# Performance work log

Measured on AMD Instinct MI355X. Metric: run time of the kernel, lower is better.

The kernel has to match this reference:

```python
import jax, jax.numpy as jnp
import numpy as np
import math

N_HEAD = 8
FACTOR = 1


def setup_inputs() -> dict:
    key = jax.random.key(0)
    kq, kk, kv = jax.random.split(key, 3)
    B, L, D = 16, 2048, 512
    return {
        "queries": jax.random.normal(kq, (B, L, D), dtype=jnp.float32),
        "keys": jax.random.normal(kk, (B, L, D), dtype=jnp.float32),
        "values": jax.random.normal(kv, (B, L, D), dtype=jnp.float32),
    }


def _autocorrelation(queries, keys, values):
    B, L, D = queries.shape
    H = N_HEAD
    E = D // H
    top_k = int(FACTOR * math.log(L))  # static: L is a Python int

    # (B,L,H,E) -> (B,H,E,L)
    q = queries.reshape(B, L, H, E).transpose(0, 2, 3, 1)
    k = keys.reshape(B, L, H, E).transpose(0, 2, 3, 1)
    v = values.reshape(B, L, H, E).transpose(0, 2, 3, 1)

    # period-based dependencies via FFT cross-correlation
    qf = jnp.fft.rfft(q, axis=-1)
    kf = jnp.fft.rfft(k, axis=-1)
    corr = jnp.fft.irfft(qf * jnp.conj(kf), n=L, axis=-1)  # (B,H,E,L)

    # time-delay aggregation (training path)
    mean_value = corr.mean(axis=(1, 2))                      # (B,L)
    index = jax.lax.top_k(mean_value.mean(axis=0), top_k)[1]  # (top_k,)
    weights = mean_value[:, index]                            # (B,top_k)
    tmp_corr = jax.nn.softmax(weights, axis=-1)               # (B,top_k)

    # roll values by each top-k delay and combine with softmax weights
    patterns = jax.vmap(lambda d: jnp.roll(v, -d, axis=-1))(index)  # (k,B,H,E,L)
    V = jnp.einsum('kbhel,bk->bhel', patterns, tmp_corr)            # (B,H,E,L)

    out = V.transpose(0, 3, 1, 2).reshape(B, L, D)
    corr_out = corr.transpose(0, 3, 1, 2).reshape(B, L, D)
    return out, corr_out


def reference(queries, keys, values):
    return _autocorrelation(queries, keys, values)
```

## Files before the change

kernel.cpp:

```cpp
#include <hip/hip_runtime.h>
#include <math.h>

#define B_  16
#define L_  2048
#define D_  512
#define K_  7
#define Q_  (B_*L_*D_)

__global__ __launch_bounds__(256) void kA(const float* __restrict__ q,
                                          const float* __restrict__ k,
                                          float* __restrict__ qT,
                                          float* __restrict__ kT) {
  __shared__ float tq[32][33];
  __shared__ float tk[32][33];
  const int l0 = blockIdx.x * 32, d0 = blockIdx.y * 32, b = blockIdx.z;
  const int tx = threadIdx.x, ty = threadIdx.y;
  const size_t ibase = (size_t)b * L_ * D_;
#pragma unroll
  for (int j = 0; j < 4; ++j) {
    const int l = l0 + ty + 8 * j;
    tq[ty + 8 * j][tx] = q[ibase + (size_t)l * D_ + d0 + tx];
    tk[ty + 8 * j][tx] = k[ibase + (size_t)l * D_ + d0 + tx];
  }
  __syncthreads();
  const size_t obase = (size_t)b * D_ * L_;
#pragma unroll
  for (int j = 0; j < 4; ++j) {
    const int d = d0 + ty + 8 * j;
    qT[obase + (size_t)d * L_ + l0 + tx] = tq[tx][ty + 8 * j];
    kT[obase + (size_t)d * L_ + l0 + tx] = tk[tx][ty + 8 * j];
  }
}

struct cf { float r, i; };
__device__ __forceinline__ cf cadd(cf a, cf b){ return {a.r+b.r, a.i+b.i}; }
__device__ __forceinline__ cf csub(cf a, cf b){ return {a.r-b.r, a.i-b.i}; }
__device__ __forceinline__ cf cmul(cf a, cf b){ return {a.r*b.r - a.i*b.i, a.r*b.i + a.i*b.r}; }
template<bool INV> __device__ __forceinline__ cf rot90(cf x){
  return INV ? cf{-x.i, x.r} : cf{x.i, -x.r};
}
__device__ __forceinline__ int swzA(int a){ return a ^ (((a >> 6) & 7) << 3); }
__device__ __forceinline__ int swzB(int a){ return a ^ (((a >> 3) ^ (a >> 6)) & 7); }

template<bool INV>
__device__ __forceinline__ void dft8(cf a[8], cf b[8]) {
  const float H = 0.70710678118654752440f;
  cf t0 = cadd(a[0],a[4]), t1 = cadd(a[1],a[5]), t2 = cadd(a[2],a[6]), t3 = cadd(a[3],a[7]);
  cf u0 = csub(a[0],a[4]), u1 = csub(a[1],a[5]), u2 = csub(a[2],a[6]), u3 = csub(a[3],a[7]);
  const cf w1 = INV ? cf{H,  H} : cf{ H, -H};
  const cf w3 = INV ? cf{-H, H} : cf{-H, -H};
  u1 = cmul(u1, w1);
  u2 = rot90<INV>(u2);
  u3 = cmul(u3, w3);
  { cf s0 = cadd(t0,t2), s1 = csub(t0,t2), s2 = cadd(t1,t3), s3 = rot90<INV>(csub(t1,t3));
    b[0]=cadd(s0,s2); b[4]=csub(s0,s2); b[2]=cadd(s1,s3); b[6]=csub(s1,s3); }
  { cf s0 = cadd(u0,u2), s1 = csub(u0,u2), s2 = cadd(u1,u3), s3 = rot90<INV>(csub(u1,u3));
    b[1]=cadd(s0,s2); b[5]=csub(s0,s2); b[3]=cadd(s1,s3); b[7]=csub(s1,s3); }
}

template<int LOG2S, bool INV, bool SRC_A>
__device__ __forceinline__ void pass8(const float* __restrict__ sr,
                                      const float* __restrict__ si,
                                      float* __restrict__ dr,
                                      float* __restrict__ di, int tid) {
  const int p = tid >> LOG2S;
  cf a[8], b[8];
#pragma unroll
  for (int l = 0; l < 8; ++l) {
    const int ix = tid + (l << 8);
    const int rs = SRC_A ? swzA(ix) : swzB(ix);
    a[l].r = sr[rs]; a[l].i = si[rs];
  }
  dft8<INV>(a, b);
  const float ANG = -0.0030679615757712823f;
  float sn, cs;
  __sincosf(ANG * (float)(p << LOG2S), &sn, &cs);
  if (INV) sn = -sn;
  const cf w1{cs, sn};
  cf w = w1;
  b[1] = cmul(b[1], w);
#pragma unroll
  for (int k = 2; k < 8; ++k) { w = cmul(w, w1); b[k] = cmul(b[k], w); }
  const int wb = tid + 7 * (p << LOG2S);
#pragma unroll
  for (int k = 0; k < 8; ++k) {
    const int ix = wb + (k << LOG2S);
    const int ws = SRC_A ? swzB(ix) : swzA(ix);
    dr[ws] = b[k].r; di[ws] = b[k].i;
  }
}

template<bool INV>
__device__ __forceinline__ void pass4_final(const float* __restrict__ sr,
                                            const float* __restrict__ si,
                                            float* __restrict__ dr,
                                            float* __restrict__ di, int tid) {
#pragma unroll
  for (int h = 0; h < 2; ++h) {
    const int j = tid + (h << 8);
    const int r0 = swzB(j), r1 = swzB(j + 512), r2 = swzB(j + 1024), r3 = swzB(j + 1536);
    cf a0{sr[r0], si[r0]}, a1{sr[r1], si[r1]}, a2{sr[r2], si[r2]}, a3{sr[r3], si[r3]};
    cf s0 = cadd(a0,a2), s1 = csub(a0,a2), s2 = cadd(a1,a3), s3 = rot90<INV>(csub(a1,a3));
    cf o0 = cadd(s0,s2), o1 = cadd(s1,s3), o2 = csub(s0,s2), o3 = csub(s1,s3);
    const int w0 = swzA(j), w1x = swzA(j + 512), w2x = swzA(j + 1024), w3x = swzA(j + 1536);
    dr[w0]  = o0.r; di[w0]  = o0.i;
    dr[w1x] = o1.r; di[w1x] = o1.i;
    dr[w2x] = o2.r; di[w2x] = o2.i;
    dr[w3x] = o3.r; di[w3x] = o3.i;
  }
}

__global__ __launch_bounds__(256) void kB(const float* __restrict__ qT,
                                          const float* __restrict__ kT,
                                          float* __restrict__ corrT) {
  __shared__ float Ar[L_], Ai[L_], Br[L_], Bi[L_];
  const int tid = threadIdx.x;
  const size_t row = (size_t)blockIdx.x * L_;

  const float4* q4 = (const float4*)(qT + row);
  const float4* k4 = (const float4*)(kT + row);
#pragma unroll
  for (int u = 0; u < 2; ++u) {
    const int idx = tid + (u << 8);
    const float4 vq = q4[idx];
    const float4 vk = k4[idx];
    const int a = swzA(idx << 2);
    *(float4*)&Ar[a] = vq;
    *(float4*)&Ai[a] = vk;
  }
  __syncthreads();

  pass8<0, false, true >(Ar, Ai, Br, Bi, tid); __syncthreads();
  pass8<3, false, false>(Br, Bi, Ar, Ai, tid); __syncthreads();
  pass8<6, false, true >(Ar, Ai, Br, Bi, tid); __syncthreads();
  pass4_final<false>    (Br, Bi, Ar, Ai, tid); __syncthreads();

  {
    cf zf[8], zg[8];
#pragma unroll
    for (int u = 0; u < 8; ++u) {
      const int f = tid + (u << 8);
      const int g = (L_ - f) & (L_ - 1);
      const int sf = swzA(f), sg = swzA(g);
      zf[u] = {Ar[sf], Ai[sf]};
      zg[u] = {Ar[sg], Ai[sg]};
    }
    __syncthreads();
#pragma unroll
    for (int u = 0; u < 8; ++u) {
      const int f = tid + (u << 8);
      const float ar = zf[u].r, ai = zf[u].i, br = zg[u].r, bi = zg[u].i;
      const float qr = 0.5f * (ar + br), qi = 0.5f * (ai - bi);
      const float kr = 0.5f * (ai + bi), ki = 0.5f * (br - ar);
      const int sf = swzA(f);
      Ar[sf] = qr * kr + qi * ki;
      Ai[sf] = qi * kr - qr * ki;
    }
    __syncthreads();
  }

  pass8<0, true, true >(Ar, Ai, Br, Bi, tid); __syncthreads();
  pass8<3, true, false>(Br, Bi, Ar, Ai, tid); __syncthreads();
  pass8<6, true, true >(Ar, Ai, Br, Bi, tid); __syncthreads();
  pass4_final<true>     (Br, Bi, Ar, Ai, tid); __syncthreads();

  float4* c4 = (float4*)(corrT + row);
  const float inv = 1.0f / (float)L_;
#pragma unroll
  for (int u = 0; u < 2; ++u) {
    const int idx = tid + (u << 8);
    const int a = swzA(idx << 2);
    float4 vr = *(const float4*)&Ar[a];
    vr.x *= inv; vr.y *= inv; vr.z *= inv; vr.w *= inv;
    c4[idx] = vr;
  }
}

__global__ __launch_bounds__(256) void kC(const float* __restrict__ corrT,
                                          float* __restrict__ corrOut,
                                          float* __restrict__ partial) {
  __shared__ float t[32][33];
  const int t0 = blockIdx.x * 32, d0 = blockIdx.y * 32, b = blockIdx.z;
  const int tx = threadIdx.x, ty = threadIdx.y;
#pragma unroll
  for (int j = 0; j < 4; ++j) {
    const int d = d0 + ty + 8 * j;
    t[ty + 8 * j][tx] = corrT[((size_t)b * D_ + d) * L_ + t0 + tx];
  }
  __syncthreads();
#pragma unroll
  for (int j = 0; j < 4; ++j) {
    const int tt = t0 + ty + 8 * j;
    corrOut[((size_t)b * L_ + tt) * D_ + d0 + tx] = t[tx][ty + 8 * j];
  }
  if (ty == 0) {
    float s = 0.f;
#pragma unroll
    for (int i = 0; i < 32; ++i) s += t[i][tx];
    partial[((size_t)b * 16 + blockIdx.y) * L_ + t0 + tx] = s;
  }
}

__global__ __launch_bounds__(256) void kD0(const float* __restrict__ partial,
                                           float* __restrict__ g) {
  __shared__ float red[4][64];
  const int tl = threadIdx.x & 63, rg = threadIdx.x >> 6;
  const int tau = blockIdx.x * 64 + tl;
  float s = 0.f;
  for (int i = rg; i < 256; i += 4) s += partial[(size_t)i * L_ + tau];
  red[rg][tl] = s;
  __syncthreads();
  if (rg == 0) g[tau] = red[0][tl] + red[1][tl] + red[2][tl] + red[3][tl];
}

__global__ __launch_bounds__(256) void kD1(const float* __restrict__ gin,
                                           const float* __restrict__ partial,
                                           int* __restrict__ oidx,
                                           float* __restrict__ ow) {
  __shared__ float g[L_];
  __shared__ float rv[256];
  __shared__ int   ri[256];
  __shared__ int   sidx[K_];
  const int tid = threadIdx.x;
#pragma unroll
  for (int u = 0; u < 8; ++u) g[tid + u * 256] = gin[tid + u * 256];
  __syncthreads();

  for (int it = 0; it < K_; ++it) {
    float bv = -1e30f; int bix = 1 << 30;
#pragma unroll
    for (int u = 0; u < 8; ++u) {
      const int tau = tid + u * 256;
      const float vv = g[tau];
      if (vv > bv || (vv == bv && tau < bix)) { bv = vv; bix = tau; }
    }
    rv[tid] = bv; ri[tid] = bix;
    __syncthreads();
    for (int off = 128; off > 0; off >>= 1) {
      if (tid < off) {
        const float v2 = rv[tid + off]; const int i2 = ri[tid + off];
        if (v2 > rv[tid] || (v2 == rv[tid] && i2 < ri[tid])) {
          rv[tid] = v2; ri[tid] = i2;
        }
      }
      __syncthreads();
    }
    if (tid == 0) { sidx[it] = ri[0]; g[ri[0]] = -3e38f; }
    __syncthreads();
  }

  if (tid < B_) {
    const int b = tid;
    float m[K_]; float mx = -1e30f;
    for (int kk = 0; kk < K_; ++kk) {
      float s = 0.f;
      for (int dt = 0; dt < 16; ++dt)
        s += partial[((size_t)b * 16 + dt) * L_ + sidx[kk]];
      m[kk] = s * (1.0f / 512.0f);
      mx = fmaxf(mx, m[kk]);
    }
    float sum = 0.f;
    for (int kk = 0; kk < K_; ++kk) { m[kk] = expf(m[kk] - mx); sum += m[kk]; }
    const float inv = 1.0f / sum;
    for (int kk = 0; kk < K_; ++kk) ow[b * K_ + kk] = m[kk] * inv;
  }
  if (tid < K_) oidx[tid] = sidx[tid];
}

__global__ __launch_bounds__(256) void kE(const float4* __restrict__ v4,
                                          const float* __restrict__ w,
                                          const int* __restrict__ idx,
                                          float4* __restrict__ out4) {
  const int bx = blockIdx.x;
  const int b  = bx >> 10;
  const int l  = ((bx & 1023) << 1) | (threadIdx.x >> 7);
  const int j  = threadIdx.x & 127;

  float ww[K_]; int rr[K_];
#pragma unroll
  for (int kk = 0; kk < K_; ++kk) {
    ww[kk] = w[b * K_ + kk];
    int r = l + idx[kk];
    if (r >= L_) r -= L_;
    rr[kk] = r;
  }
  const size_t vb = (size_t)b * L_ * 128;
  float4 acc = make_float4(0.f, 0.f, 0.f, 0.f);
#pragma unroll
  for (int kk = 0; kk < K_; ++kk) {
    const float4 vv = v4[vb + (size_t)rr[kk] * 128 + j];
    acc.x += ww[kk] * vv.x; acc.y += ww[kk] * vv.y;
    acc.z += ww[kk] * vv.z; acc.w += ww[kk] * vv.w;
  }
  out4[vb + (size_t)l * 128 + j] = acc;
}

extern "C" void kernel_launch(void* const* d_in, const int* in_sizes, int n_in,
                              void* d_out, int out_size, void* d_ws, size_t ws_size,
                              hipStream_t stream) {
  const float* q = (const float*)d_in[0];
  const float* k = (const float*)d_in[1];
  const float* v = (const float*)d_in[2];

  float* out     = (float*)d_out;
  float* corrOut = out + Q_;
  float* qT = out;
  float* kT = corrOut;

  float* corrT   = (float*)d_ws;
  float* partial = corrT + Q_;
  int*   oidx    = (int*)(partial + (size_t)B_ * 16 * L_);
  float* ow      = (float*)(oidx + 16);
  float* g2048   = corrT;

  const dim3 thr(32, 8);
  kA<<<dim3(L_ / 32, D_ / 32, B_), thr, 0, stream>>>(q, k, qT, kT);
  kB<<<B_ * D_, 256, 0, stream>>>(qT, kT, corrT);
  kC<<<dim3(L_ / 32, D_ / 32, B_), thr, 0, stream>>>(corrT, corrOut, partial);
  kD0<<<32, 256, 0, stream>>>(partial, g2048);
  kD1<<<1, 256, 0, stream>>>(g2048, partial, oidx, ow);
  kE<<<(B_ * L_) / 2, 256, 0, stream>>>((const float4*)v, ow, oidx, (float4*)out);
}
```

Measured before the change: 207.1 us.

## Pack two channels' correlation spectra into one inverse FFT per block

Each FFT block now handles two channels. It runs two forward complex FFTs, each packing q and k as real and imaginary parts. It then combines the two real cross-spectra S1 + i*S2 into one Hermitian-free complex spectrum, so a single inverse FFT yields both correlation rows as its real and imaginary outputs. This removes one of the four FFTs per channel pair. Shared memory also moves to interleaved float2 with a single new XOR swizzle. The cost is extra shared memory (S1 buffer), fewer blocks, and a serial dependency across the two forward FFTs in a block.

```diff
diff --git a/kernel.cpp b/kernel.cpp
--- a/kernel.cpp
+++ b/kernel.cpp
@@ -39,8 +39,13 @@
 template<bool INV> __device__ __forceinline__ cf rot90(cf x){
   return INV ? cf{-x.i, x.r} : cf{x.i, -x.r};
 }
-__device__ __forceinline__ int swzA(int a){ return a ^ (((a >> 6) & 7) << 3); }
-__device__ __forceinline__ int swzB(int a){ return a ^ (((a >> 3) ^ (a >> 6)) & 7); }
+__device__ __forceinline__ int swz(int a){ return a ^ (((a >> 4) ^ (a >> 8)) & 15); }
+__device__ __forceinline__ cf ldx(const float2* __restrict__ p, int i){
+  const float2 v = p[swz(i)]; return {v.x, v.y};
+}
+__device__ __forceinline__ void stx(float2* __restrict__ p, int i, cf v){
+  p[swz(i)] = {v.r, v.i};
+}
 
 template<bool INV>
 __device__ __forceinline__ void dft8(cf a[8], cf b[8]) {
@@ -58,19 +63,13 @@
     b[1]=cadd(s0,s2); b[5]=csub(s0,s2); b[3]=cadd(s1,s3); b[7]=csub(s1,s3); }
 }
 
-template<int LOG2S, bool INV, bool SRC_A>
-__device__ __forceinline__ void pass8(const float* __restrict__ sr,
-                                      const float* __restrict__ si,
-                                      float* __restrict__ dr,
-                                      float* __restrict__ di, int tid) {
+template<int LOG2S, bool INV>
+__device__ __forceinline__ void pass8f2(const float2* __restrict__ src,
+                                        float2* __restrict__ dst, int tid) {
   const int p = tid >> LOG2S;
   cf a[8], b[8];
 #pragma unroll
-  for (int l = 0; l < 8; ++l) {
-    const int ix = tid + (l << 8);
-    const int rs = SRC_A ? swzA(ix) : swzB(ix);
-    a[l].r = sr[rs]; a[l].i = si[rs];
-  }
+  for (int l = 0; l < 8; ++l) a[l] = ldx(src, tid + (l << 8));
   dft8<INV>(a, b);
   const float ANG = -0.0030679615757712823f;
   float sn, cs;
@@ -83,97 +82,128 @@
   for (int k = 2; k < 8; ++k) { w = cmul(w, w1); b[k] = cmul(b[k], w); }
   const int wb = tid + 7 * (p << LOG2S);
 #pragma unroll
-  for (int k = 0; k < 8; ++k) {
-    const int ix = wb + (k << LOG2S);
-    const int ws = SRC_A ? swzB(ix) : swzA(ix);
-    dr[ws] = b[k].r; di[ws] = b[k].i;
-  }
+  for (int k = 0; k < 8; ++k) stx(dst, wb + (k << LOG2S), b[k]);
 }
 
 template<bool INV>
-__device__ __forceinline__ void pass4_final(const float* __restrict__ sr,
-                                            const float* __restrict__ si,
-                                            float* __restrict__ dr,
-                                            float* __restrict__ di, int tid) {
+__device__ __forceinline__ void pass4f2(const float2* __restrict__ src,
+                                        float2* __restrict__ dst, int tid) {
 #pragma unroll
   for (int h = 0; h < 2; ++h) {
     const int j = tid + (h << 8);
-    const int r0 = swzB(j), r1 = swzB(j + 512), r2 = swzB(j + 1024), r3 = swzB(j + 1536);
-    cf a0{sr[r0], si[r0]}, a1{sr[r1], si[r1]}, a2{sr[r2], si[r2]}, a3{sr[r3], si[r3]};
+    cf a0 = ldx(src, j), a1 = ldx(src, j + 512), a2 = ldx(src, j + 1024), a3 = ldx(src, j + 1536);
     cf s0 = cadd(a0,a2), s1 = csub(a0,a2), s2 = cadd(a1,a3), s3 = rot90<INV>(csub(a1,a3));
-    cf o0 = cadd(s0,s2), o1 = cadd(s1,s3), o2 = csub(s0,s2), o3 = csub(s1,s3);
-    const int w0 = swzA(j), w1x = swzA(j + 512), w2x = swzA(j + 1024), w3x = swzA(j + 1536);
-    dr[w0]  = o0.r; di[w0]  = o0.i;
-    dr[w1x] = o1.r; di[w1x] = o1.i;
-    dr[w2x] = o2.r; di[w2x] = o2.i;
-    dr[w3x] = o3.r; di[w3x] = o3.i;
+    stx(dst, j,        cadd(s0,s2));
+    stx(dst, j + 512,  cadd(s1,s3));
+    stx(dst, j + 1024, csub(s0,s2));
+    stx(dst, j + 1536, csub(s1,s3));
+  }
+}
+
+__device__ __forceinline__ void load_ch(const float* __restrict__ qp,
+                                        const float* __restrict__ kp,
+                                        float2* __restrict__ A, int tid) {
+#pragma unroll
+  for (int u = 0; u < 2; ++u) {
+    const int i4 = tid + (u << 8);
+    const float4 vq = ((const float4*)qp)[i4];
+    const float4 vk = ((const float4*)kp)[i4];
+    const int base = i4 << 2;
+    A[swz(base + 0)] = {vq.x, vk.x};
+    A[swz(base + 1)] = {vq.y, vk.y};
+    A[swz(base + 2)] = {vq.z, vk.z};
+    A[swz(base + 3)] = {vq.w, vk.w};
+  }
+}
+
+__device__ __forceinline__ void spectrum_half(const float2* __restrict__ A,
+                                              float2* __restrict__ S1, int tid) {
+#pragma unroll
+  for (int u = 0; u < 4; ++u) {
+    const int f = tid + (u << 8);
+    if (f == 0) {
+      const cf z0 = ldx(A, 0), zn = ldx(A, 1024);
+      S1[0] = {z0.r * z0.i, zn.r * zn.i};
+    } else {
+      const cf a = ldx(A, f), b = ldx(A, 2048 - f);
+      const float qr = 0.5f * (a.r + b.r), qi = 0.5f * (a.i - b.i);
+      const float kr = 0.5f * (a.i + b.i), ki = 0.5f * (b.r - a.r);
+      S1[f] = {qr * kr + qi * ki, qi * kr - qr * ki};
+    }
+  }
+}
+
+__device__ __forceinline__ void combine(const float2* __restrict__ A,
+                                        const float2* __restrict__ S1,
+                                        float2* __restrict__ dst, int tid) {
+#pragma unroll
+  for (int u = 0; u < 4; ++u) {
+    const int f = tid + (u << 8);
+    if (f == 0) {
+      const cf z0 = ldx(A, 0), zn = ldx(A, 1024);
+      const float s2_0 = z0.r * z0.i, s2_n = zn.r * zn.i;
+      const float2 s1 = S1[0];
+      stx(dst, 0,    {s1.x, s2_0});
+      stx(dst, 1024, {s1.y, s2_n});
+    } else {
+      const cf a = ldx(A, f), b = ldx(A, 2048 - f);
+      const float qr = 0.5f * (a.r + b.r), qi = 0.5f * (a.i - b.i);
+      const float kr = 0.5f * (a.i + b.i), ki = 0.5f * (b.r - a.r);
+      const float s2r = qr * kr + qi * ki, s2i = qi * kr - qr * ki;
+      const float2 s1 = S1[f];
+      stx(dst, f,        {s1.x - s2i,  s1.y + s2r});
+      stx(dst, 2048 - f, {s1.x + s2i, -s1.y + s2r});
+    }
+  }
+}
+
+__device__ __forceinline__ void store2(const float2* __restrict__ Bb,
+                                       float* __restrict__ c0,
+                                       float* __restrict__ c1, int tid) {
+  const float inv = 1.0f / (float)L_;
+#pragma unroll
+  for (int u = 0; u < 2; ++u) {
+    const int i4 = tid + (u << 8);
+    const int base = i4 << 2;
+    const float2 z0 = Bb[swz(base + 0)];
+    const float2 z1 = Bb[swz(base + 1)];
+    const float2 z2 = Bb[swz(base + 2)];
+    const float2 z3 = Bb[swz(base + 3)];
+    ((float4*)c0)[i4] = make_float4(z0.x*inv, z1.x*inv, z2.x*inv, z3.x*inv);
+    ((float4*)c1)[i4] = make_float4(z0.y*inv, z1.y*inv, z2.y*inv, z3.y*inv);
   }
 }
 
 __global__ __launch_bounds__(256) void kB(const float* __restrict__ qT,
                                           const float* __restrict__ kT,
                                           float* __restrict__ corrT) {
-  __shared__ float Ar[L_], Ai[L_], Br[L_], Bi[L_];
+  __shared__ float2 A[L_];
+  __shared__ float2 Bb[L_];
+  __shared__ float2 S1[L_ / 2];
   const int tid = threadIdx.x;
-  const size_t row = (size_t)blockIdx.x * L_;
-
-  const float4* q4 = (const float4*)(qT + row);
-  const float4* k4 = (const float4*)(kT + row);
-#pragma unroll
-  for (int u = 0; u < 2; ++u) {
-    const int idx = tid + (u << 8);
-    const float4 vq = q4[idx];
-    const float4 vk = k4[idx];
-    const int a = swzA(idx << 2);
-    *(float4*)&Ar[a] = vq;
-    *(float4*)&Ai[a] = vk;
-  }
-  __syncthreads();
-
-  pass8<0, false, true >(Ar, Ai, Br, Bi, tid); __syncthreads();
-  pass8<3, false, false>(Br, Bi, Ar, Ai, tid); __syncthreads();
-  pass8<6, false, true >(Ar, Ai, Br, Bi, tid); __syncthreads();
-  pass4_final<false>    (Br, Bi, Ar, Ai, tid); __syncthreads();
-
-  {
-    cf zf[8], zg[8];
-#pragma unroll
-    for (int u = 0; u < 8; ++u) {
-      const int f = tid + (u << 8);
-      const int g = (L_ - f) & (L_ - 1);
-      const int sf = swzA(f), sg = swzA(g);
-      zf[u] = {Ar[sf], Ai[sf]};
-      zg[u] = {Ar[sg], Ai[sg]};
-    }
-    __syncthreads();
-#pragma unroll
-    for (int u = 0; u < 8; ++u) {
-      const int f = tid + (u << 8);
-      const float ar = zf[u].r, ai = zf[u].i, br = zg[u].r, bi = zg[u].i;
-      const float qr = 0.5f * (ar + br), qi = 0.5f * (ai - bi);
-      const float kr = 0.5f * (ai + bi), ki = 0.5f * (br - ar);
-      const int sf = swzA(f);
-      Ar[sf] = qr * kr + qi * ki;
-      Ai[sf] = qi * kr - qr * ki;
-    }
-    __syncthreads();
-  }
-
-  pass8<0, true, true >(Ar, Ai, Br, Bi, tid); __syncthreads();
-  pass8<3, true, false>(Br, Bi, Ar, Ai, tid); __syncthreads();
-  pass8<6, true, true >(Ar, Ai, Br, Bi, tid); __syncthreads();
-  pass4_final<true>     (Br, Bi, Ar, Ai, tid); __syncthreads();
-
-  float4* c4 = (float4*)(corrT + row);
-  const float inv = 1.0f / (float)L_;
-#pragma unroll
-  for (int u = 0; u < 2; ++u) {
-    const int idx = tid + (u << 8);
-    const int a = swzA(idx << 2);
-    float4 vr = *(const float4*)&Ar[a];
-    vr.x *= inv; vr.y *= inv; vr.z *= inv; vr.w *= inv;
-    c4[idx] = vr;
-  }
+  const size_t row0 = (size_t)(blockIdx.x * 2) * L_;
+  const size_t row1 = row0 + L_;
+
+  load_ch(qT + row0, kT + row0, A, tid);  __syncthreads();
+  pass8f2<0, false>(A, Bb, tid);          __syncthreads();
+  pass8f2<3, false>(Bb, A, tid);          __syncthreads();
+  pass8f2<6, false>(A, Bb, tid);          __syncthreads();
+  pass4f2<false>(Bb, A, tid);             __syncthreads();
+  spectrum_half(A, S1, tid);              __syncthreads();
+
+  load_ch(qT + row1, kT + row1, A, tid);  __syncthreads();
+  pass8f2<0, false>(A, Bb, tid);          __syncthreads();
+  pass8f2<3, false>(Bb, A, tid);          __syncthreads();
+  pass8f2<6, false>(A, Bb, tid);          __syncthreads();
+  pass4f2<false>(Bb, A, tid);             __syncthreads();
+
+  combine(A, S1, Bb, tid);                __syncthreads();
+  pass8f2<0, true>(Bb, A, tid);           __syncthreads();
+  pass8f2<3, true>(A, Bb, tid);           __syncthreads();
+  pass8f2<6, true>(Bb, A, tid);           __syncthreads();
+  pass4f2<true>(A, Bb, tid);              __syncthreads();
+
+  store2(Bb, corrT + row0, corrT + row1, tid);
 }
 
 __global__ __launch_bounds__(256) void kC(const float* __restrict__ corrT,
@@ -315,7 +345,7 @@
 
   const dim3 thr(32, 8);
   kA<<<dim3(L_ / 32, D_ / 32, B_), thr, 0, stream>>>(q, k, qT, kT);
-  kB<<<B_ * D_, 256, 0, stream>>>(qT, kT, corrT);
+  kB<<<(B_ * D_) / 2, 256, 0, stream>>>(qT, kT, corrT);
   kC<<<dim3(L_ / 32, D_ / 32, B_), thr, 0, stream>>>(corrT, corrOut, partial);
   kD0<<<32, 256, 0, stream>>>(partial, g2048);
   kD1<<<1, 256, 0, stream>>>(g2048, partial, oidx, ow);
```

Measured after the change: 217.5 us. +5.0%, slower.

## Batch four channels per FFT block and pack two inverse FFTs per complex transform

Applied to the files above, without the earlier changes.

The FFT kernel now handles four channels per 512-thread block. Each forward complex FFT still packs q and k as real and imaginary parts, and two channels' cross-spectra are merged into one complex inverse FFT whose real and imaginary outputs give the two correlations. This cuts the inverse FFT work in half. Shared memory moves to interleaved float2 with a new XOR swizzle. In exchange it uses more shared memory per block (5×16KB), adds extra barriers, and forward passes run twice in sequence.

```diff
diff --git a/kernel.cpp b/kernel.cpp
--- a/kernel.cpp
+++ b/kernel.cpp
@@ -39,8 +39,13 @@
 template<bool INV> __device__ __forceinline__ cf rot90(cf x){
   return INV ? cf{-x.i, x.r} : cf{x.i, -x.r};
 }
-__device__ __forceinline__ int swzA(int a){ return a ^ (((a >> 6) & 7) << 3); }
-__device__ __forceinline__ int swzB(int a){ return a ^ (((a >> 3) ^ (a >> 6)) & 7); }
+__device__ __forceinline__ int swz(int a){ return a ^ (((a >> 4) ^ (a >> 8)) & 15); }
+__device__ __forceinline__ cf ldx(const float2* __restrict__ p, int i){
+  const float2 v = p[swz(i)]; return {v.x, v.y};
+}
+__device__ __forceinline__ void stx(float2* __restrict__ p, int i, cf v){
+  p[swz(i)] = {v.r, v.i};
+}
 
 template<bool INV>
 __device__ __forceinline__ void dft8(cf a[8], cf b[8]) {
@@ -58,19 +63,13 @@
     b[1]=cadd(s0,s2); b[5]=csub(s0,s2); b[3]=cadd(s1,s3); b[7]=csub(s1,s3); }
 }
 
-template<int LOG2S, bool INV, bool SRC_A>
-__device__ __forceinline__ void pass8(const float* __restrict__ sr,
-                                      const float* __restrict__ si,
-                                      float* __restrict__ dr,
-                                      float* __restrict__ di, int tid) {
-  const int p = tid >> LOG2S;
+template<int LOG2S, bool INV>
+__device__ __forceinline__ void pass8f2(const float2* __restrict__ src,
+                                        float2* __restrict__ dst, int j) {
+  const int p = j >> LOG2S;
   cf a[8], b[8];
 #pragma unroll
-  for (int l = 0; l < 8; ++l) {
-    const int ix = tid + (l << 8);
-    const int rs = SRC_A ? swzA(ix) : swzB(ix);
-    a[l].r = sr[rs]; a[l].i = si[rs];
-  }
+  for (int l = 0; l < 8; ++l) a[l] = ldx(src, j + (l << 8));
   dft8<INV>(a, b);
   const float ANG = -0.0030679615757712823f;
   float sn, cs;
@@ -81,99 +80,124 @@
   b[1] = cmul(b[1], w);
 #pragma unroll
   for (int k = 2; k < 8; ++k) { w = cmul(w, w1); b[k] = cmul(b[k], w); }
-  const int wb = tid + 7 * (p << LOG2S);
-#pragma unroll
-  for (int k = 0; k < 8; ++k) {
-    const int ix = wb + (k << LOG2S);
-    const int ws = SRC_A ? swzB(ix) : swzA(ix);
-    dr[ws] = b[k].r; di[ws] = b[k].i;
-  }
+  const int wb = j + 7 * (p << LOG2S);
+#pragma unroll
+  for (int k = 0; k < 8; ++k) stx(dst, wb + (k << LOG2S), b[k]);
 }
 
 template<bool INV>
-__device__ __forceinline__ void pass4_final(const float* __restrict__ sr,
-                                            const float* __restrict__ si,
-                                            float* __restrict__ dr,
-                                            float* __restrict__ di, int tid) {
+__device__ __forceinline__ void pass4f2(const float2* __restrict__ src,
+                                        float2* __restrict__ dst, int j) {
 #pragma unroll
   for (int h = 0; h < 2; ++h) {
-    const int j = tid + (h << 8);
-    const int r0 = swzB(j), r1 = swzB(j + 512), r2 = swzB(j + 1024), r3 = swzB(j + 1536);
-    cf a0{sr[r0], si[r0]}, a1{sr[r1], si[r1]}, a2{sr[r2], si[r2]}, a3{sr[r3], si[r3]};
+    const int jj = j + (h << 8);
+    cf a0 = ldx(src, jj), a1 = ldx(src, jj + 512), a2 = ldx(src, jj + 1024), a3 = ldx(src, jj + 1536);
     cf s0 = cadd(a0,a2), s1 = csub(a0,a2), s2 = cadd(a1,a3), s3 = rot90<INV>(csub(a1,a3));
-    cf o0 = cadd(s0,s2), o1 = cadd(s1,s3), o2 = csub(s0,s2), o3 = csub(s1,s3);
-    const int w0 = swzA(j), w1x = swzA(j + 512), w2x = swzA(j + 1024), w3x = swzA(j + 1536);
-    dr[w0]  = o0.r; di[w0]  = o0.i;
-    dr[w1x] = o1.r; di[w1x] = o1.i;
-    dr[w2x] = o2.r; di[w2x] = o2.i;
-    dr[w3x] = o3.r; di[w3x] = o3.i;
-  }
-}
-
-__global__ __launch_bounds__(256) void kB(const float* __restrict__ qT,
-                                          const float* __restrict__ kT,
-                                          float* __restrict__ corrT) {
-  __shared__ float Ar[L_], Ai[L_], Br[L_], Bi[L_];
-  const int tid = threadIdx.x;
-  const size_t row = (size_t)blockIdx.x * L_;
-
-  const float4* q4 = (const float4*)(qT + row);
-  const float4* k4 = (const float4*)(kT + row);
+    stx(dst, jj,        cadd(s0,s2));
+    stx(dst, jj + 512,  cadd(s1,s3));
+    stx(dst, jj + 1024, csub(s0,s2));
+    stx(dst, jj + 1536, csub(s1,s3));
+  }
+}
+
+__device__ __forceinline__ void loadch(const float* __restrict__ qp,
+                                       const float* __restrict__ kp,
+                                       float2* __restrict__ Z, int j) {
+  const float4* q4 = (const float4*)qp;
+  const float4* k4 = (const float4*)kp;
 #pragma unroll
   for (int u = 0; u < 2; ++u) {
-    const int idx = tid + (u << 8);
-    const float4 vq = q4[idx];
-    const float4 vk = k4[idx];
-    const int a = swzA(idx << 2);
-    *(float4*)&Ar[a] = vq;
-    *(float4*)&Ai[a] = vk;
-  }
-  __syncthreads();
-
-  pass8<0, false, true >(Ar, Ai, Br, Bi, tid); __syncthreads();
-  pass8<3, false, false>(Br, Bi, Ar, Ai, tid); __syncthreads();
-  pass8<6, false, true >(Ar, Ai, Br, Bi, tid); __syncthreads();
-  pass4_final<false>    (Br, Bi, Ar, Ai, tid); __syncthreads();
-
-  {
-    cf zf[8], zg[8];
-#pragma unroll
-    for (int u = 0; u < 8; ++u) {
-      const int f = tid + (u << 8);
-      const int g = (L_ - f) & (L_ - 1);
-      const int sf = swzA(f), sg = swzA(g);
-      zf[u] = {Ar[sf], Ai[sf]};
-      zg[u] = {Ar[sg], Ai[sg]};
+    const int g = j + (u << 8);
+    const float4 vq = q4[g];
+    const float4 vk = k4[g];
+    const int base = g << 2;
+    Z[swz(base + 0)] = {vq.x, vk.x};
+    Z[swz(base + 1)] = {vq.y, vk.y};
+    Z[swz(base + 2)] = {vq.z, vk.z};
+    Z[swz(base + 3)] = {vq.w, vk.w};
+  }
+}
+
+__device__ __forceinline__ void combine2(const float2* __restrict__ Za,
+                                         const float2* __restrict__ Zb,
+                                         float2* __restrict__ Zo, int t) {
+#pragma unroll
+  for (int u = 0; u < 2; ++u) {
+    const int f = t + (u << 9);
+    if (f == 0) {
+      const cf a0 = ldx(Za, 0), an = ldx(Za, 1024);
+      const cf b0 = ldx(Zb, 0), bn = ldx(Zb, 1024);
+      stx(Zo, 0,    {a0.r * a0.i, b0.r * b0.i});
+      stx(Zo, 1024, {an.r * an.i, bn.r * bn.i});
+    } else {
+      const cf a = ldx(Za, f), am = ldx(Za, 2048 - f);
+      const float aqr = 0.5f * (a.r + am.r), aqi = 0.5f * (a.i - am.i);
+      const float akr = 0.5f * (a.i + am.i), aki = 0.5f * (am.r - a.r);
+      const float sar = aqr * akr + aqi * aki, sai = aqi * akr - aqr * aki;
+      const cf b = ldx(Zb, f), bm = ldx(Zb, 2048 - f);
+      const float bqr = 0.5f * (b.r + bm.r), bqi = 0.5f * (b.i - bm.i);
+      const float bkr = 0.5f * (b.i + bm.i), bki = 0.5f * (bm.r - b.r);
+      const float sbr = bqr * bkr + bqi * bki, sbi = bqi * bkr - bqr * bki;
+      stx(Zo, f,        {sar - sbi,  sai + sbr});
+      stx(Zo, 2048 - f, {sar + sbi, -sai + sbr});
     }
-    __syncthreads();
-#pragma unroll
-    for (int u = 0; u < 8; ++u) {
-      const int f = tid + (u << 8);
-      const float ar = zf[u].r, ai = zf[u].i, br = zg[u].r, bi = zg[u].i;
-      const float qr = 0.5f * (ar + br), qi = 0.5f * (ai - bi);
-      const float kr = 0.5f * (ai + bi), ki = 0.5f * (br - ar);
-      const int sf = swzA(f);
-      Ar[sf] = qr * kr + qi * ki;
-      Ai[sf] = qi * kr - qr * ki;
-    }
-    __syncthreads();
-  }
-
-  pass8<0, true, true >(Ar, Ai, Br, Bi, tid); __syncthreads();
-  pass8<3, true, false>(Br, Bi, Ar, Ai, tid); __syncthreads();
-  pass8<6, true, true >(Ar, Ai, Br, Bi, tid); __syncthreads();
-  pass4_final<true>     (Br, Bi, Ar, Ai, tid); __syncthreads();
-
-  float4* c4 = (float4*)(corrT + row);
+  }
+}
+
+__device__ __forceinline__ void storepair(const float2* __restrict__ Z,
+                                          float* __restrict__ c0,
+                                          float* __restrict__ c1, int j) {
   const float inv = 1.0f / (float)L_;
 #pragma unroll
   for (int u = 0; u < 2; ++u) {
-    const int idx = tid + (u << 8);
-    const int a = swzA(idx << 2);
-    float4 vr = *(const float4*)&Ar[a];
-    vr.x *= inv; vr.y *= inv; vr.z *= inv; vr.w *= inv;
-    c4[idx] = vr;
-  }
+    const int g = j + (u << 8);
+    const int base = g << 2;
+    const float2 z0 = Z[swz(base + 0)];
+    const float2 z1 = Z[swz(base + 1)];
+    const float2 z2 = Z[swz(base + 2)];
+    const float2 z3 = Z[swz(base + 3)];
+    ((float4*)c0)[g] = make_float4(z0.x*inv, z1.x*inv, z2.x*inv, z3.x*inv);
+    ((float4*)c1)[g] = make_float4(z0.y*inv, z1.y*inv, z2.y*inv, z3.y*inv);
+  }
+}
+
+__global__ __launch_bounds__(512, 4) void kB(const float* __restrict__ qT,
+                                             const float* __restrict__ kT,
+                                             float* __restrict__ corrT) {
+  __shared__ float2 U0[L_], U1[L_], U2[L_], U3[L_], U4[L_];
+  const int t  = threadIdx.x;
+  const int ch = t >> 8;
+  const int j  = t & 255;
+  const size_t base = (size_t)blockIdx.x * 4 * L_;
+
+  float2* ZD = ch ? U1 : U0;
+  float2* ZS = ch ? U3 : U2;
+
+  loadch(qT + base + (size_t)ch * L_, kT + base + (size_t)ch * L_, ZD, j);
+  __syncthreads();
+  pass8f2<0, false>(ZD, ZS, j); __syncthreads();
+  pass8f2<3, false>(ZS, ZD, j); __syncthreads();
+  pass8f2<6, false>(ZD, ZS, j); __syncthreads();
+  pass4f2<false>(ZS, ZD, j);    __syncthreads();
+  combine2(U0, U1, U4, t);      __syncthreads();
+
+  loadch(qT + base + (size_t)(ch + 2) * L_, kT + base + (size_t)(ch + 2) * L_, ZD, j);
+  __syncthreads();
+  pass8f2<0, false>(ZD, ZS, j); __syncthreads();
+  pass8f2<3, false>(ZS, ZD, j); __syncthreads();
+  pass8f2<6, false>(ZD, ZS, j); __syncthreads();
+  pass4f2<false>(ZS, ZD, j);    __syncthreads();
+  combine2(U0, U1, U2, t);      __syncthreads();
+
+  float2* Sp = ch ? U2 : U4;
+  float2* Tp = ch ? U1 : U0;
+  pass8f2<0, true>(Sp, Tp, j);  __syncthreads();
+  pass8f2<3, true>(Tp, Sp, j);  __syncthreads();
+  pass8f2<6, true>(Sp, Tp, j);  __syncthreads();
+  pass4f2<true>(Tp, Sp, j);     __syncthreads();
+
+  storepair(Sp, corrT + base + (size_t)(2 * ch) * L_,
+                corrT + base + (size_t)(2 * ch + 1) * L_, j);
 }
 
 __global__ __launch_bounds__(256) void kC(const float* __restrict__ corrT,
@@ -315,7 +339,7 @@
 
   const dim3 thr(32, 8);
   kA<<<dim3(L_ / 32, D_ / 32, B_), thr, 0, stream>>>(q, k, qT, kT);
-  kB<<<B_ * D_, 256, 0, stream>>>(qT, kT, corrT);
+  kB<<<(B_ * D_) / 4, 512, 0, stream>>>(qT, kT, corrT);
   kC<<<dim3(L_ / 32, D_ / 32, B_), thr, 0, stream>>>(corrT, corrOut, partial);
   kD0<<<32, 256, 0, stream>>>(partial, g2048);
   kD1<<<1, 256, 0, stream>>>(g2048, partial, oidx, ow);
```

New measurement: 336.8 us. 62.6% more time.
